# Optimization experiments

Measured on AMD Instinct MI355X. Metric: run time of the kernel, lower is better.

Reference implementation:

```python
import math
import jax, jax.numpy as jnp
import numpy as np

B, S, H = 2, 2048, 1024
NH = 16
HD = H // NH            # 64
ROT = int(HD * 0.25)    # 16
QKV_SLOTS = 1024
PROJ_SLOTS = 1024
FFN_SLOTS = 4096
EPS = 1e-5


def gelu_l2_norm(x, axis=-1):
    # F.gelu (exact erf) then L2-normalize and rescale by sqrt(dim)
    g = jax.nn.gelu(x, approximate=False)
    n = jnp.linalg.norm(g, ord=2, axis=axis, keepdims=True)
    return g / n * math.sqrt(g.shape[axis])


def layer_norm(x, w, b):
    mu = jnp.mean(x, axis=-1, keepdims=True)
    var = jnp.mean(jnp.square(x - mu), axis=-1, keepdims=True)
    return (x - mu) * jax.lax.rsqrt(var + EPS) * w + b


def pattention(x, key_tok, val_tok):
    # [.., in] @ [slots, in]^T -> [.., slots]; NOTE: scale MULTIPLIES (as in source)
    aw = jnp.einsum('bsh,ph->bsp', x, key_tok) * math.sqrt(x.shape[-1])
    aw = gelu_l2_norm(aw, axis=-1)
    return jnp.einsum('bsp,pd->bsd', aw, val_tok)


def rotary_cos_sin(seq_len, rot_dim, base=10000.0):
    inv_freq = 1.0 / (base ** (jnp.arange(0, rot_dim, 2, dtype=jnp.float32) / rot_dim))
    t = jnp.arange(seq_len, dtype=jnp.float32)
    freqs = jnp.einsum('s,d->sd', t, inv_freq)           # [S, rot/2]
    emb = jnp.concatenate([freqs, freqs], axis=-1)       # [S, rot]
    return jnp.cos(emb), jnp.sin(emb)


def rotate_half(x):
    x1, x2 = jnp.split(x, 2, axis=-1)
    return jnp.concatenate([-x2, x1], axis=-1)


def setup_inputs() -> dict:
    key = jax.random.key(0)
    ks = jax.random.split(key, 12)
    p = lambda k, shape: jax.random.normal(k, shape, dtype=jnp.float32) * 0.02
    return {
        'x': jax.random.normal(ks[0], (B, S, H), dtype=jnp.float32),
        'ln1_w': jnp.ones((H,), jnp.float32), 'ln1_b': jnp.zeros((H,), jnp.float32),
        'ln2_w': jnp.ones((H,), jnp.float32), 'ln2_b': jnp.zeros((H,), jnp.float32),
        'q_key': p(ks[1], (QKV_SLOTS, H)), 'q_val': p(ks[2], (QKV_SLOTS, H)),
        'k_key': p(ks[3], (QKV_SLOTS, H)), 'k_val': p(ks[4], (QKV_SLOTS, H)),
        'v_key': p(ks[5], (QKV_SLOTS, H)), 'v_val': p(ks[6], (QKV_SLOTS, H)),
        'proj_key': p(ks[7], (PROJ_SLOTS, H)), 'proj_val': p(ks[8], (PROJ_SLOTS, H)),
        'ffn_key': p(ks[9], (FFN_SLOTS, H)), 'ffn_val': p(ks[10], (FFN_SLOTS, H)),
    }


def reference(x, ln1_w, ln1_b, ln2_w, ln2_b, q_key, q_val, k_key, k_val,
              v_key, v_val, proj_key, proj_val, ffn_key, ffn_val):
    residual = x
    xn = layer_norm(x, ln1_w, ln1_b)
    q = pattention(xn, q_key, q_val).reshape(B, S, NH, HD)
    k = pattention(xn, k_key, k_val).reshape(B, S, NH, HD)
    v = pattention(xn, v_key, v_val).reshape(B, S, NH, HD)

    cos, sin = rotary_cos_sin(S, ROT)          # [S, ROT]
    cos = cos[None, :, None, :]
    sin = sin[None, :, None, :]
    q_rot, q_pass = q[..., :ROT], q[..., ROT:]
    k_rot, k_pass = k[..., :ROT], k[..., ROT:]
    q_rot = q_rot * cos + rotate_half(q_rot) * sin
    k_rot = k_rot * cos + rotate_half(k_rot) * sin
    q = jnp.concatenate([q_rot, q_pass], axis=-1).transpose(0, 2, 1, 3)  # [B,NH,S,HD]
    k = jnp.concatenate([k_rot, k_pass], axis=-1).transpose(0, 2, 1, 3)
    v = v.transpose(0, 2, 1, 3)

    scale = math.sqrt(HD)
    causal = jnp.triu(jnp.ones((S, S), dtype=bool), k=1)
    attn_mask = jnp.where(causal, jnp.float32(-10000.0), jnp.float32(0.0))
    aw = jnp.einsum('bhqd,bhkd->bhqk', q, k) / scale + attn_mask
    aw = gelu_l2_norm(aw, axis=-1)
    o = jnp.einsum('bhqk,bhkd->bhqd', aw, v)
    o = o.transpose(0, 2, 1, 3).reshape(B, S, H)

    x = residual + pattention(o, proj_key, proj_val)
    residual = x
    x = residual + pattention(layer_norm(x, ln2_w, ln2_b), ffn_key, ffn_val)
    return x
```

## Files before the change

kernel.cpp:

```cpp
#include <hip/hip_runtime.h>

typedef __bf16 bf16x8 __attribute__((ext_vector_type(8)));
typedef float f32x4 __attribute__((ext_vector_type(4)));
typedef unsigned short u16;

__device__ __forceinline__ float b2f(u16 u) {
  union { unsigned int i; float f; } v; v.i = ((unsigned int)u) << 16; return v.f;
}
__device__ __forceinline__ u16 f2b(float f) {
  union { float f; unsigned int i; } v; v.f = f;
  unsigned int x = v.i;
  x += 0x7fffu + ((x >> 16) & 1u);
  return (u16)(x >> 16);
}
__device__ __forceinline__ float gelu_f(float x) {
  float x2 = x * x;
  float p = x * (1.5957691216f + 0.0713548162f * x2);
  float e = __expf(p);
  float r = __builtin_amdgcn_rcpf(1.0f + e);
  return x - x * r;
}
__device__ __forceinline__ void async16(const u16* g, u16* l) {
  __builtin_amdgcn_global_load_lds(
      (const __attribute__((address_space(1))) void*)g,
      (__attribute__((address_space(3))) void*)l, 16, 0, 0);
}
__device__ __forceinline__ void swz(int& bn, int& bm, int& bz) {
  int gx = (int)gridDim.x, gy = (int)gridDim.y;
  int flat = (int)(blockIdx.x + gridDim.x * (blockIdx.y + gridDim.y * blockIdx.z));
  int seq = flat >> 3;
  int nbm = gy >> 3;
  bm = (flat & 7) * nbm + seq % nbm;
  int rest = seq / nbm;
  bn = rest % gx;
  bz = rest / gx;
}

union U4 { uint4 u; u16 s[8]; };
union PF { bf16x8 v; u16 s[8]; };

__global__ __launch_bounds__(256) void cvt9_kernel(
    const float* __restrict__ qk, const float* __restrict__ kk,
    const float* __restrict__ vk, const float* __restrict__ pk,
    const float* __restrict__ fk, u16* __restrict__ w, float* __restrict__ ssqz) {
  int z = blockIdx.y;
  int i = blockIdx.x * 256 + threadIdx.x;
  if (z == 8) {
    if (i < 20480) ssqz[i] = 0.f;
    return;
  }
  const float* in = (z == 0) ? qk : (z == 1) ? kk : (z == 2) ? vk : (z == 3) ? pk
                    : fk + (size_t)(z - 4) * 1048576;
  u16* o = w + (size_t)z * 1048576;
  float4 f = ((const float4*)in)[i];
  ushort4 s;
  s.x = f2b(f.x); s.y = f2b(f.y); s.z = f2b(f.z); s.w = f2b(f.w);
  ((ushort4*)o)[i] = s;
}

__global__ __launch_bounds__(256) void cvtT8_kernel(
    const float* __restrict__ qv, const float* __restrict__ kv,
    const float* __restrict__ vv, const float* __restrict__ pv,
    const float* __restrict__ fv, u16* __restrict__ valsT, u16* __restrict__ fvT) {
  __shared__ float t[32][33];
  int z = blockIdx.z;
  const float* in; u16* o; int Rout, rowoff;
  if (z < 4) {
    in = (z == 0) ? qv : (z == 1) ? kv : (z == 2) ? vv : pv;
    o = valsT + (size_t)z * 1048576; Rout = 1024; rowoff = 0;
  } else {
    in = fv + (size_t)(z - 4) * 1048576;
    o = fvT; Rout = 4096; rowoff = (z - 4) * 1024;
  }
  int bc = blockIdx.x, br = blockIdx.y;
  int tid = threadIdx.x;
  int r = tid >> 5, cc = tid & 31;
  #pragma unroll
  for (int i = 0; i < 4; ++i)
    t[r + i * 8][cc] = in[(size_t)(br * 32 + r + i * 8) * 1024 + bc * 32 + cc];
  __syncthreads();
  #pragma unroll
  for (int i = 0; i < 4; ++i)
    o[(size_t)(bc * 32 + r + i * 8) * Rout + rowoff + br * 32 + cc] = f2b(t[cc][r + i * 8]);
}

__global__ __launch_bounds__(256) void ln_kernel(const float* __restrict__ x,
    const float* __restrict__ w, const float* __restrict__ b, u16* __restrict__ out) {
  int wv = threadIdx.x >> 6, lane = threadIdx.x & 63;
  int row = blockIdx.x * 4 + wv;
  const float* xr = x + (size_t)row * 1024;
  float4 v[4];
  float s = 0.f, s2 = 0.f;
  #pragma unroll
  for (int i = 0; i < 4; ++i) {
    v[i] = ((const float4*)xr)[lane + 64 * i];
    s += v[i].x + v[i].y + v[i].z + v[i].w;
    s2 += v[i].x * v[i].x + v[i].y * v[i].y + v[i].z * v[i].z + v[i].w * v[i].w;
  }
  #pragma unroll
  for (int m = 1; m < 64; m <<= 1) { s += __shfl_xor(s, m); s2 += __shfl_xor(s2, m); }
  float mu = s * (1.0f / 1024.0f);
  float inv = rsqrtf(s2 * (1.0f / 1024.0f) - mu * mu + 1e-5f);
  u16* orow = out + (size_t)row * 1024;
  #pragma unroll
  for (int i = 0; i < 4; ++i) {
    int c = (lane + 64 * i) * 4;
    ushort4 o;
    o.x = f2b((v[i].x - mu) * inv * w[c]     + b[c]);
    o.y = f2b((v[i].y - mu) * inv * w[c + 1] + b[c + 1]);
    o.z = f2b((v[i].z - mu) * inv * w[c + 2] + b[c + 2]);
    o.w = f2b((v[i].w - mu) * inv * w[c + 3] + b[c + 3]);
    ((ushort4*)orow)[lane + 64 * i] = o;
  }
}

template <int TM>
__global__ __launch_bounds__(256) void gemm_key(
    const u16* __restrict__ A, size_t sAz,
    const u16* __restrict__ B, size_t sBz,
    u16* __restrict__ C, size_t sCz,
    float* __restrict__ ssqb, size_t sSz,
    int N, int K, float alpha) {
  constexpr int AI = TM / 32;
  __shared__ __align__(16) u16 As[2][TM * 32];
  __shared__ __align__(16) u16 Bs[2][128 * 32];
  int bn, bm, bz;
  swz(bn, bm, bz);
  const u16* Ab = A + (size_t)bz * sAz + (size_t)bm * TM * K;
  const u16* Bb = B + (size_t)bz * sBz + (size_t)bn * 128 * K;
  int tid = threadIdx.x, lane = tid & 63, wv = tid >> 6;
  int quad = lane >> 4, l16 = lane & 15;
  int lr = lane >> 2, lc = (lane & 3) * 8;
  int wm = wv >> 1, wn = wv & 1;
  int RB = wm * (TM / 2), CB = wn * 64;
  f32x4 zero = {0.f, 0.f, 0.f, 0.f};
  f32x4 acc[AI][4];
  #pragma unroll
  for (int i = 0; i < AI; ++i)
    #pragma unroll
    for (int j = 0; j < 4; ++j) acc[i][j] = zero;
  #pragma unroll
  for (int t = 0; t < TM / 64; ++t) {
    int ia = wv * (TM / 64) + t;
    async16(Ab + (size_t)(ia * 16 + lr) * K + lc, &As[0][ia * 512]);
  }
  #pragma unroll
  for (int t = 0; t < 2; ++t) {
    int ib = wv * 2 + t;
    async16(Bb + (size_t)(ib * 16 + lr) * K + lc, &Bs[0][ib * 512]);
  }
  for (int k0 = 0, cur = 0; k0 < K; k0 += 32, cur ^= 1) {
    __syncthreads();
    if (k0 + 32 < K) {
      #pragma unroll
      for (int t = 0; t < TM / 64; ++t) {
        int ia = wv * (TM / 64) + t;
        async16(Ab + (size_t)(ia * 16 + lr) * K + k0 + 32 + lc, &As[cur ^ 1][ia * 512]);
      }
      #pragma unroll
      for (int t = 0; t < 2; ++t) {
        int ib = wv * 2 + t;
        async16(Bb + (size_t)(ib * 16 + lr) * K + k0 + 32 + lc, &Bs[cur ^ 1][ib * 512]);
      }
    }
    bf16x8 af[AI], bf[4];
    #pragma unroll
    for (int i = 0; i < AI; ++i)
      af[i] = *(const bf16x8*)&As[cur][(RB + i * 16 + l16) * 32 + quad * 8];
    #pragma unroll
    for (int j = 0; j < 4; ++j)
      bf[j] = *(const bf16x8*)&Bs[cur][(CB + j * 16 + l16) * 32 + quad * 8];
    #pragma unroll
    for (int i = 0; i < AI; ++i)
      #pragma unroll
      for (int j = 0; j < 4; ++j)
        acc[i][j] = __builtin_amdgcn_mfma_f32_16x16x32_bf16(af[i], bf[j], acc[i][j], 0, 0, 0);
  }
  #pragma unroll
  for (int i = 0; i < AI; ++i) {
    int rbase = bm * TM + RB + i * 16 + quad * 4;
    float srow[4] = {0.f, 0.f, 0.f, 0.f};
    #pragma unroll
    for (int j = 0; j < 4; ++j) {
      int c = bn * 128 + CB + j * 16 + l16;
      #pragma unroll
      for (int reg = 0; reg < 4; ++reg) {
        float g = gelu_f(acc[i][j][reg] * alpha);
        srow[reg] += g * g;
        C[(size_t)bz * sCz + (size_t)(rbase + reg) * N + c] = f2b(g);
      }
    }
    #pragma unroll
    for (int reg = 0; reg < 4; ++reg) {
      float s = srow[reg];
      s += __shfl_xor(s, 1); s += __shfl_xor(s, 2);
      s += __shfl_xor(s, 4); s += __shfl_xor(s, 8);
      if (l16 == 0) atomicAdd(&ssqb[bz * sSz + rbase + reg], s);
    }
  }
}

template <int TM, int MODE, bool ROT>
__global__ __launch_bounds__(256) void gemm_val(
    const u16* __restrict__ A, size_t sAz,
    const u16* __restrict__ B, size_t sBz,
    void* __restrict__ C, size_t sCz,
    const float* __restrict__ ssqb, size_t sSz,
    int N, int K, int kzs, int klen, float sqrtP, const float* __restrict__ res) {
  constexpr int AI = TM / 32;
  __shared__ __align__(16) u16 As[2][TM * 32];
  __shared__ __align__(16) u16 Bs[2][128 * 32];
  int bn, bm, bz;
  swz(bn, bm, bz);
  const u16* Ab = A + (size_t)bz * sAz + (size_t)bm * TM * K;
  const u16* Bb = B + (size_t)bz * sBz + (size_t)bn * 128 * K;
  int tid = threadIdx.x, lane = tid & 63, wv = tid >> 6;
  int quad = lane >> 4, l16 = lane & 15;
  int lr = lane >> 2, lc = (lane & 3) * 8;
  int wm = wv >> 1, wn = wv & 1;
  int RB = wm * (TM / 2), CB = wn * 64;
  f32x4 zero = {0.f, 0.f, 0.f, 0.f};
  f32x4 acc[AI][4];
  #pragma unroll
  for (int i = 0; i < AI; ++i)
    #pragma unroll
    for (int j = 0; j < 4; ++j) acc[i][j] = zero;
  int kb0 = bz * kzs;
  #pragma unroll
  for (int t = 0; t < TM / 64; ++t) {
    int ia = wv * (TM / 64) + t;
    async16(Ab + (size_t)(ia * 16 + lr) * K + kb0 + lc, &As[0][ia * 512]);
  }
  #pragma unroll
  for (int t = 0; t < 2; ++t) {
    int ib = wv * 2 + t;
    async16(Bb + (size_t)(ib * 16 + lr) * K + kb0 + lc, &Bs[0][ib * 512]);
  }
  for (int k0 = kb0, cur = 0; k0 < kb0 + klen; k0 += 32, cur ^= 1) {
    __syncthreads();
    if (k0 + 32 < kb0 + klen) {
      #pragma unroll
      for (int t = 0; t < TM / 64; ++t) {
        int ia = wv * (TM / 64) + t;
        async16(Ab + (size_t)(ia * 16 + lr) * K + k0 + 32 + lc, &As[cur ^ 1][ia * 512]);
      }
      #pragma unroll
      for (int t = 0; t < 2; ++t) {
        int ib = wv * 2 + t;
        async16(Bb + (size_t)(ib * 16 + lr) * K + k0 + 32 + lc, &Bs[cur ^ 1][ib * 512]);
      }
    }
    bf16x8 af[AI], bf[4];
    #pragma unroll
    for (int i = 0; i < AI; ++i)
      af[i] = *(const bf16x8*)&As[cur][(RB + i * 16 + l16) * 32 + quad * 8];
    #pragma unroll
    for (int j = 0; j < 4; ++j)
      bf[j] = *(const bf16x8*)&Bs[cur][(CB + j * 16 + l16) * 32 + quad * 8];
    #pragma unroll
    for (int i = 0; i < AI; ++i)
      #pragma unroll
      for (int j = 0; j < 4; ++j)
        acc[i][j] = __builtin_amdgcn_mfma_f32_16x16x32_bf16(af[i], bf[j], acc[i][j], 0, 0, 0);
  }
  #pragma unroll
  for (int i = 0; i < AI; ++i) {
    int rbase = bm * TM + RB + i * 16 + quad * 4;
    float sc[4];
    if (MODE < 2) {
      #pragma unroll
      for (int reg = 0; reg < 4; ++reg)
        sc[reg] = sqrtP * rsqrtf(ssqb[bz * sSz + rbase + reg]);
    }
    #pragma unroll
    for (int j = 0; j < 4; ++j) {
      int c = bn * 128 + CB + j * 16 + l16;
      #pragma unroll
      for (int reg = 0; reg < 4; ++reg) {
        float v = acc[i][j][reg];
        size_t idx = (size_t)(rbase + reg) * N + c;
        if (MODE == 0) {
          float vs = v * sc[reg];
          if (ROT && j == 0) {
            float prt = __shfl_xor(vs, 8);
            if (bz < 2) {
              int seq = (rbase + reg) & 2047;
              float fr = exp2f((float)(l16 & 7) * -1.66096404744368f);
              float ang = (float)seq * fr;
              float c_ = __cosf(ang), s_ = __sinf(ang);
              vs = (l16 < 8) ? (vs * c_ - prt * s_) : (vs * c_ + prt * s_);
            }
          }
          ((u16*)C)[(size_t)bz * sCz + idx] = f2b(vs);
        } else if (MODE == 1) {
          ((float*)C)[idx] = v * sc[reg] + res[idx];
        } else {
          ((float*)C)[(size_t)bz * sCz + idx] = v;
        }
      }
    }
  }
}

__global__ __launch_bounds__(256) void vt_kernel(const u16* __restrict__ vb,
                                                 u16* __restrict__ vT) {
  __shared__ __align__(16) u16 T[64][72];
  int st = blockIdx.x, bh = blockIdx.y;
  int b = bh >> 4, h = bh & 15;
  int tid = threadIdx.x;
  #pragma unroll
  for (int i = 0; i < 2; ++i) {
    int l = tid + 256 * i;
    int s = l >> 3, dc = l & 7;
    *(uint4*)&T[s][dc * 8] =
        *(const uint4*)(vb + (size_t)(b * 2048 + st * 64 + s) * 1024 + h * 64 + dc * 8);
  }
  __syncthreads();
  #pragma unroll
  for (int i = 0; i < 2; ++i) {
    int l = tid + 256 * i;
    int d = l >> 3, scid = l & 7;
    int blk = (scid >> 2) * 32;
    int qq = (scid & 3) * 4;
    U4 u;
    #pragma unroll
    for (int j = 0; j < 8; ++j)
      u.s[j] = T[blk + (j >> 2) * 16 + qq + (j & 3)][d];
    *(uint4*)(vT + ((size_t)bh * 64 + d) * 2048 + st * 64 + scid * 8) = u.u;
  }
}

__global__ __launch_bounds__(256) void attn_kernel(
    const u16* __restrict__ qb, const u16* __restrict__ kb,
    const u16* __restrict__ vT, u16* __restrict__ ob) {
  __shared__ __align__(16) u16 Qs[64 * 64];
  __shared__ __align__(16) u16 Ks[2][64 * 64];
  __shared__ __align__(16) u16 Vts[2][64 * 64];
  int bh = blockIdx.x;
  int qt = 31 - (int)blockIdx.y;
  int b = bh >> 4, h = bh & 15;
  const u16* qp = qb + (size_t)b * 2048 * 1024 + h * 64;
  const u16* kp = kb + (size_t)b * 2048 * 1024 + h * 64;
  const u16* vp = vT + (size_t)bh * 64 * 2048;
  int tid = threadIdx.x, lane = tid & 63, wv = tid >> 6;
  int quad = lane >> 4, l16 = lane & 15;
  int lr8 = lane >> 3, lc8 = (lane & 7) * 8;
  int MR = wv * 16;
  int nkt = qt + 1;
  #pragma unroll
  for (int t = 0; t < 2; ++t) {
    int idx = wv * 2 + t;
    async16(qp + (size_t)(qt * 64 + idx * 8 + lr8) * 1024 + lc8, &Qs[idx * 512]);
    async16(kp + (size_t)(idx * 8 + lr8) * 1024 + lc8, &Ks[0][idx * 512]);
    async16(vp + (size_t)(idx * 8 + lr8) * 2048 + lc8, &Vts[0][idx * 512]);
  }
  f32x4 zero = {0.f, 0.f, 0.f, 0.f};
  f32x4 oacc[4];
  #pragma unroll
  for (int dn = 0; dn < 4; ++dn) oacc[dn] = zero;
  float ssql = 0.f;
  bf16x8 bq0 = {}, bq1 = {};
  for (int kt = 0, cur = 0; kt < nkt; ++kt, cur ^= 1) {
    __syncthreads();
    if (kt == 0) {
      bq0 = *(const bf16x8*)&Qs[(MR + l16) * 64 + quad * 8];
      bq1 = *(const bf16x8*)&Qs[(MR + l16) * 64 + 32 + quad * 8];
    }
    if (kt + 1 < nkt) {
      #pragma unroll
      for (int t = 0; t < 2; ++t) {
        int idx = wv * 2 + t;
        async16(kp + (size_t)((kt + 1) * 64 + idx * 8 + lr8) * 1024 + lc8, &Ks[cur ^ 1][idx * 512]);
        async16(vp + (size_t)(idx * 8 + lr8) * 2048 + (kt + 1) * 64 + lc8, &Vts[cur ^ 1][idx * 512]);
      }
    }
    bool dg = (kt == qt);
    #pragma unroll
    for (int kc = 0; kc < 2; ++kc) {
      PF pf;
      #pragma unroll
      for (int snh = 0; snh < 2; ++snh) {
        int sn = kc * 2 + snh;
        bf16x8 ak0 = *(const bf16x8*)&Ks[cur][(sn * 16 + l16) * 64 + quad * 8];
        bf16x8 ak1 = *(const bf16x8*)&Ks[cur][(sn * 16 + l16) * 64 + 32 + quad * 8];
        f32x4 st = zero;
        st = __builtin_amdgcn_mfma_f32_16x16x32_bf16(ak0, bq0, st, 0, 0, 0);
        st = __builtin_amdgcn_mfma_f32_16x16x32_bf16(ak1, bq1, st, 0, 0, 0);
        #pragma unroll
        for (int r = 0; r < 4; ++r) {
          float gl = gelu_f(st[r] * 0.125f);
          if (dg && (sn * 16 + quad * 4 + r > MR + l16)) gl = 0.f;
          ssql += gl * gl;
          pf.s[snh * 4 + r] = f2b(gl);
        }
      }
      #pragma unroll
      for (int dn = 0; dn < 4; ++dn) {
        bf16x8 bv = *(const bf16x8*)&Vts[cur][(dn * 16 + l16) * 64 + kc * 32 + quad * 8];
        oacc[dn] = __builtin_amdgcn_mfma_f32_16x16x32_bf16(pf.v, bv, oacc[dn], 0, 0, 0);
      }
    }
  }
  ssql += __shfl_xor(ssql, 16);
  ssql += __shfl_xor(ssql, 32);
  float sc = 45.254834f * rsqrtf(ssql);
  #pragma unroll
  for (int dn = 0; dn < 4; ++dn)
    #pragma unroll
    for (int r = 0; r < 4; ++r) {
      float scr = __shfl(sc, quad * 4 + r);
      int row = qt * 64 + MR + quad * 4 + r;
      int col = h * 64 + dn * 16 + l16;
      ob[(size_t)(b * 2048 + row) * 1024 + col] = f2b(oacc[dn][r] * scr);
    }
}

__global__ __launch_bounds__(256) void fin_kernel(
    const float* __restrict__ p0, const float* __restrict__ p1,
    const float* __restrict__ x1, const float* __restrict__ ssqf,
    float* __restrict__ out) {
  int row = blockIdx.x, t = threadIdx.x;
  float s = 64.0f * rsqrtf(ssqf[row]);
  size_t base = (size_t)row * 1024 + t * 4;
  float4 a = *(const float4*)(p0 + base);
  float4 b = *(const float4*)(p1 + base);
  float4 r = *(const float4*)(x1 + base);
  float4 o;
  o.x = r.x + s * (a.x + b.x); o.y = r.y + s * (a.y + b.y);
  o.z = r.z + s * (a.z + b.z); o.w = r.w + s * (a.w + b.w);
  *(float4*)(out + base) = o;
}

extern "C" void kernel_launch(void* const* d_in, const int* in_sizes, int n_in,
                              void* d_out, int out_size, void* d_ws, size_t ws_size,
                              hipStream_t stream) {
  const float* x    = (const float*)d_in[0];
  const float* ln1w = (const float*)d_in[1];
  const float* ln1b = (const float*)d_in[2];
  const float* ln2w = (const float*)d_in[3];
  const float* ln2b = (const float*)d_in[4];
  const float* qk   = (const float*)d_in[5];
  const float* qv   = (const float*)d_in[6];
  const float* kk   = (const float*)d_in[7];
  const float* kv   = (const float*)d_in[8];
  const float* vk   = (const float*)d_in[9];
  const float* vv   = (const float*)d_in[10];
  const float* pk   = (const float*)d_in[11];
  const float* pv   = (const float*)d_in[12];
  const float* fk   = (const float*)d_in[13];
  const float* fv   = (const float*)d_in[14];
  float* out = (float*)d_out;

  const size_t M1 = 1048576;
  u16* w = (u16*)d_ws;
  u16* wkeys  = w;
  u16* wpk    = w + 3 * M1;
  u16* wfk    = w + 4 * M1;
  u16* wvalsT = w + 8 * M1;
  u16* wpvT   = w + 11 * M1;
  u16* wfvT   = w + 12 * M1;
  u16* xn     = w + 16 * M1;
  u16* gq     = w + 20 * M1;
  u16* ob     = w + 20 * M1;
  u16* vT     = w + 24 * M1;
  u16* gp     = w + 28 * M1;
  u16* gf     = w + 20 * M1;
  u16* qb     = w + 36 * M1;
  u16* kb     = w + 40 * M1;
  u16* vb     = w + 44 * M1;
  float* ssq_qkv  = (float*)(w + 48 * M1);
  float* ssq_proj = ssq_qkv + 12288;
  float* ssq_ffn  = ssq_qkv + 16384;
  float* x1 = (float*)(w + 52 * M1);
  float* p0 = (float*)w;
  float* p1 = (float*)(w + 36 * M1);

  dim3 blk(256);
  cvt9_kernel<<<dim3(1024, 9), blk, 0, stream>>>(qk, kk, vk, pk, fk, w, ssq_qkv);
  cvtT8_kernel<<<dim3(32, 32, 8), blk, 0, stream>>>(qv, kv, vv, pv, fv, wvalsT, wfvT);

  ln_kernel<<<1024, blk, 0, stream>>>(x, ln1w, ln1b, xn);
  gemm_key<128><<<dim3(8, 32, 3), blk, 0, stream>>>(
      xn, 0, wkeys, M1, gq, 4 * M1, ssq_qkv, 4096, 1024, 1024, 32.0f);
  gemm_val<128, 0, true><<<dim3(8, 32, 3), blk, 0, stream>>>(
      gq, 4 * M1, wvalsT, M1, qb, 4 * M1, ssq_qkv, 4096, 1024, 1024, 0, 1024, 32.0f, nullptr);

  vt_kernel<<<dim3(32, 32), blk, 0, stream>>>(vb, vT);
  attn_kernel<<<dim3(32, 32), blk, 0, stream>>>(qb, kb, vT, ob);

  gemm_key<64><<<dim3(8, 64, 1), blk, 0, stream>>>(
      ob, 0, wpk, 0, gp, 0, ssq_proj, 0, 1024, 1024, 32.0f);
  gemm_val<64, 1, false><<<dim3(8, 64, 1), blk, 0, stream>>>(
      gp, 0, wpvT, 0, x1, 0, ssq_proj, 0, 1024, 1024, 0, 1024, 32.0f, x);

  ln_kernel<<<1024, blk, 0, stream>>>(x1, ln2w, ln2b, xn);
  gemm_key<128><<<dim3(32, 32, 1), blk, 0, stream>>>(
      xn, 0, wfk, 0, gf, 0, ssq_ffn, 0, 4096, 1024, 32.0f);
  gemm_val<128, 2, false><<<dim3(8, 32, 2), blk, 0, stream>>>(
      gf, 0, wfvT, 0, p0, 18 * M1, ssq_ffn, 0, 1024, 4096, 2048, 2048, 0.0f, nullptr);
  fin_kernel<<<4096, blk, 0, stream>>>(p0, p1, x1, ssq_ffn, out);
}
```

Measured before the change: 447.8 us.

## Add 256x256-tile 8-wave pipelined GEMM for QKV and FFN key projections

Adds a new gemm8 kernel with 256x256 output tiles, 512 threads and double-buffered async global-to-LDS loads. It splits each K-step into four MFMA phases, interleaving the loads with compute under barriers and setprio. It replaces the QKV key/value GEMMs and the FFN key GEMM, carrying the gelu/sum-of-squares and rotary/normalisation epilogues along. The aim is more data reuse per tile and better overlap of memory with MFMA work. The trade-off is fewer blocks, which lowers occupancy and can hurt load balance for the smaller grids (192 blocks for QKV).

New measurement: 444.1 us. Within noise of the previous version (-0.8%).

```diff
diff --git a/kernel.cpp b/kernel.cpp
--- a/kernel.cpp
+++ b/kernel.cpp
@@ -111,6 +111,193 @@
     o.z = f2b((v[i].z - mu) * inv * w[c + 2] + b[c + 2]);
     o.w = f2b((v[i].w - mu) * inv * w[c + 3] + b[c + 3]);
     ((ushort4*)orow)[lane + 64 * i] = o;
+  }
+}
+
+__device__ __forceinline__ bf16x8 ldfrag(const u16* __restrict__ base, int row, int ks, int quad) {
+  int off = (row * 64 + ks * 32 + quad * 8) ^ ((row & 7) << 3);
+  return *(const bf16x8*)&base[off];
+}
+
+template <int EPI, bool ROT>
+__global__ __launch_bounds__(512, 2) void gemm8(
+    const u16* __restrict__ A, size_t sAz,
+    const u16* __restrict__ B, size_t sBz,
+    u16* __restrict__ C, size_t sCz,
+    float* __restrict__ ssqb, size_t sSz,
+    int N, int K, float alpha) {
+  __shared__ __align__(16) u16 As[2][2][8192];
+  __shared__ __align__(16) u16 Bs[2][2][8192];
+  int bn, bm, bz;
+  swz(bn, bm, bz);
+  int tid = threadIdx.x, lane = tid & 63, wv = tid >> 6;
+  int quad = lane >> 4, l16 = lane & 15;
+  int wm = wv >> 2, wn = wv & 3;
+  const u16* Ab = A + (size_t)bz * sAz + (size_t)(bm * 256) * K;
+  const u16* Bb = B + (size_t)bz * sBz + (size_t)(bn * 256) * K;
+  size_t off0, off1;
+  {
+    int r0 = wv * 16 + (lane >> 3);
+    int r1 = r0 + 8;
+    off0 = (size_t)r0 * K + ((lane & 7) ^ (r0 & 7)) * 8;
+    off1 = (size_t)r1 * K + ((lane & 7) ^ (r1 & 7)) * 8;
+  }
+  int lds0 = wv * 1024, lds1 = wv * 1024 + 512;
+  const size_t hK = (size_t)128 * K;
+  auto STAGE = [&](const u16* gb, int k0, u16* lds) {
+    async16(gb + off0 + k0, lds + lds0);
+    async16(gb + off1 + k0, lds + lds1);
+  };
+
+  f32x4 zero = {0.f, 0.f, 0.f, 0.f};
+  f32x4 acc[8][4];
+  #pragma unroll
+  for (int i = 0; i < 8; ++i)
+    #pragma unroll
+    for (int j = 0; j < 4; ++j) acc[i][j] = zero;
+
+  int NT = K >> 6;
+  STAGE(Bb,      0, &Bs[0][0][0]);
+  STAGE(Bb + hK, 0, &Bs[0][1][0]);
+  STAGE(Ab,      0, &As[0][0][0]);
+  STAGE(Ab + hK, 0, &As[0][1][0]);
+  STAGE(Bb,      64, &Bs[1][0][0]);
+  STAGE(Bb + hK, 64, &Bs[1][1][0]);
+  STAGE(Ab,      64, &As[1][0][0]);
+  asm volatile("s_waitcnt vmcnt(6)" ::: "memory");
+  __builtin_amdgcn_sched_barrier(0);
+  __builtin_amdgcn_s_barrier();
+
+  bf16x8 a[4][2], b[4][2];
+  int brow = (wn & 1) * 64;
+  for (int t = 0; t < NT; ++t) {
+    int cur = t & 1;
+    const u16* Ar = &As[cur][wm][0];
+    const u16* Br = &Bs[cur][wn >> 1][0];
+    #pragma unroll
+    for (int j = 0; j < 4; ++j)
+      #pragma unroll
+      for (int ks = 0; ks < 2; ++ks)
+        b[j][ks] = ldfrag(Br, brow + j * 16 + l16, ks, quad);
+    #pragma unroll
+    for (int i = 0; i < 4; ++i)
+      #pragma unroll
+      for (int ks = 0; ks < 2; ++ks)
+        a[i][ks] = ldfrag(Ar, i * 16 + l16, ks, quad);
+    if (t + 1 < NT) STAGE(Ab + hK, (t + 1) * 64, &As[cur ^ 1][1][0]);
+    __builtin_amdgcn_s_barrier();
+    asm volatile("s_waitcnt lgkmcnt(0)" ::: "memory");
+    __builtin_amdgcn_sched_barrier(0);
+    __builtin_amdgcn_s_setprio(1);
+    #pragma unroll
+    for (int i = 0; i < 4; ++i)
+      #pragma unroll
+      for (int j = 0; j < 2; ++j) {
+        acc[i][j] = __builtin_amdgcn_mfma_f32_16x16x32_bf16(a[i][0], b[j][0], acc[i][j], 0, 0, 0);
+        acc[i][j] = __builtin_amdgcn_mfma_f32_16x16x32_bf16(a[i][1], b[j][1], acc[i][j], 0, 0, 0);
+      }
+    __builtin_amdgcn_s_setprio(0);
+    __builtin_amdgcn_sched_barrier(0);
+    __builtin_amdgcn_s_barrier();
+    if (t + 2 < NT) STAGE(Bb, (t + 2) * 64, &Bs[cur][0][0]);
+    __builtin_amdgcn_s_barrier();
+    __builtin_amdgcn_s_setprio(1);
+    #pragma unroll
+    for (int i = 0; i < 4; ++i)
+      #pragma unroll
+      for (int j = 2; j < 4; ++j) {
+        acc[i][j] = __builtin_amdgcn_mfma_f32_16x16x32_bf16(a[i][0], b[j][0], acc[i][j], 0, 0, 0);
+        acc[i][j] = __builtin_amdgcn_mfma_f32_16x16x32_bf16(a[i][1], b[j][1], acc[i][j], 0, 0, 0);
+      }
+    __builtin_amdgcn_s_setprio(0);
+    __builtin_amdgcn_sched_barrier(0);
+    __builtin_amdgcn_s_barrier();
+    #pragma unroll
+    for (int i = 0; i < 4; ++i)
+      #pragma unroll
+      for (int ks = 0; ks < 2; ++ks)
+        a[i][ks] = ldfrag(Ar, 64 + i * 16 + l16, ks, quad);
+    if (t + 2 < NT) STAGE(Bb + hK, (t + 2) * 64, &Bs[cur][1][0]);
+    __builtin_amdgcn_s_barrier();
+    asm volatile("s_waitcnt lgkmcnt(0)" ::: "memory");
+    __builtin_amdgcn_sched_barrier(0);
+    __builtin_amdgcn_s_setprio(1);
+    #pragma unroll
+    for (int i = 0; i < 4; ++i)
+      #pragma unroll
+      for (int j = 0; j < 2; ++j) {
+        acc[4 + i][j] = __builtin_amdgcn_mfma_f32_16x16x32_bf16(a[i][0], b[j][0], acc[4 + i][j], 0, 0, 0);
+        acc[4 + i][j] = __builtin_amdgcn_mfma_f32_16x16x32_bf16(a[i][1], b[j][1], acc[4 + i][j], 0, 0, 0);
+      }
+    __builtin_amdgcn_s_setprio(0);
+    __builtin_amdgcn_sched_barrier(0);
+    __builtin_amdgcn_s_barrier();
+    if (t + 2 < NT) STAGE(Ab, (t + 2) * 64, &As[cur][0][0]);
+    __builtin_amdgcn_s_barrier();
+    __builtin_amdgcn_s_setprio(1);
+    #pragma unroll
+    for (int i = 0; i < 4; ++i)
+      #pragma unroll
+      for (int j = 2; j < 4; ++j) {
+        acc[4 + i][j] = __builtin_amdgcn_mfma_f32_16x16x32_bf16(a[i][0], b[j][0], acc[4 + i][j], 0, 0, 0);
+        acc[4 + i][j] = __builtin_amdgcn_mfma_f32_16x16x32_bf16(a[i][1], b[j][1], acc[4 + i][j], 0, 0, 0);
+      }
+    __builtin_amdgcn_s_setprio(0);
+    if (t < NT - 1) {
+      if (t == NT - 2) asm volatile("s_waitcnt vmcnt(0)" ::: "memory");
+      else             asm volatile("s_waitcnt vmcnt(6)" ::: "memory");
+    }
+    __builtin_amdgcn_sched_barrier(0);
+    __builtin_amdgcn_s_barrier();
+  }
+
+  #pragma unroll
+  for (int i = 0; i < 8; ++i) {
+    int rbase = bm * 256 + wm * 128 + i * 16 + quad * 4;
+    if (EPI == 0) {
+      float srow[4] = {0.f, 0.f, 0.f, 0.f};
+      #pragma unroll
+      for (int j = 0; j < 4; ++j) {
+        int c = bn * 256 + wn * 64 + j * 16 + l16;
+        #pragma unroll
+        for (int reg = 0; reg < 4; ++reg) {
+          float g = gelu_f(acc[i][j][reg] * alpha);
+          srow[reg] += g * g;
+          C[(size_t)bz * sCz + (size_t)(rbase + reg) * N + c] = f2b(g);
+        }
+      }
+      #pragma unroll
+      for (int reg = 0; reg < 4; ++reg) {
+        float s = srow[reg];
+        s += __shfl_xor(s, 1); s += __shfl_xor(s, 2);
+        s += __shfl_xor(s, 4); s += __shfl_xor(s, 8);
+        if (l16 == 0) atomicAdd(&ssqb[bz * sSz + rbase + reg], s);
+      }
+    } else {
+      float sc[4];
+      #pragma unroll
+      for (int reg = 0; reg < 4; ++reg)
+        sc[reg] = alpha * rsqrtf(ssqb[bz * sSz + rbase + reg]);
+      #pragma unroll
+      for (int j = 0; j < 4; ++j) {
+        int c = bn * 256 + wn * 64 + j * 16 + l16;
+        #pragma unroll
+        for (int reg = 0; reg < 4; ++reg) {
+          float vs = acc[i][j][reg] * sc[reg];
+          if (ROT && j == 0) {
+            float prt = __shfl_xor(vs, 8);
+            if (bz < 2) {
+              int seq = (rbase + reg) & 2047;
+              float fr = exp2f((float)(l16 & 7) * -1.66096404744368f);
+              float ang = (float)seq * fr;
+              float c_ = __cosf(ang), s_ = __sinf(ang);
+              vs = (l16 < 8) ? (vs * c_ - prt * s_) : (vs * c_ + prt * s_);
+            }
+          }
+          C[(size_t)bz * sCz + (size_t)(rbase + reg) * N + c] = f2b(vs);
+        }
+      }
+    }
   }
 }
 
@@ -480,10 +667,10 @@
   cvtT8_kernel<<<dim3(32, 32, 8), blk, 0, stream>>>(qv, kv, vv, pv, fv, wvalsT, wfvT);
 
   ln_kernel<<<1024, blk, 0, stream>>>(x, ln1w, ln1b, xn);
-  gemm_key<128><<<dim3(8, 32, 3), blk, 0, stream>>>(
+  gemm8<0, false><<<dim3(4, 16, 3), 512, 0, stream>>>(
       xn, 0, wkeys, M1, gq, 4 * M1, ssq_qkv, 4096, 1024, 1024, 32.0f);
-  gemm_val<128, 0, true><<<dim3(8, 32, 3), blk, 0, stream>>>(
-      gq, 4 * M1, wvalsT, M1, qb, 4 * M1, ssq_qkv, 4096, 1024, 1024, 0, 1024, 32.0f, nullptr);
+  gemm8<1, true><<<dim3(4, 16, 3), 512, 0, stream>>>(
+      gq, 4 * M1, wvalsT, M1, qb, 4 * M1, ssq_qkv, 4096, 1024, 1024, 32.0f);
 
   vt_kernel<<<dim3(32, 32), blk, 0, stream>>>(vb, vT);
   attn_kernel<<<dim3(32, 32), blk, 0, stream>>>(qb, kb, vT, ob);
@@ -494,7 +681,7 @@
       gp, 0, wpvT, 0, x1, 0, ssq_proj, 0, 1024, 1024, 0, 1024, 32.0f, x);
 
   ln_kernel<<<1024, blk, 0, stream>>>(x1, ln2w, ln2b, xn);
-  gemm_key<128><<<dim3(32, 32, 1), blk, 0, stream>>>(
+  gemm8<0, false><<<dim3(16, 16, 1), 512, 0, stream>>>(
       xn, 0, wfk, 0, gf, 0, ssq_ffn, 0, 4096, 1024, 32.0f);
   gemm_val<128, 2, false><<<dim3(8, 32, 2), blk, 0, stream>>>(
       gf, 0, wfvT, 0, p0, 18 * M1, ssq_ffn, 0, 1024, 4096, 2048, 2048, 0.0f, nullptr);
```
